# Kernel tuning notes

Measured on AMD Instinct MI355X. Metric: run time of the kernel, lower is better.

## Reference

```python
import jax, jax.numpy as jnp
import numpy as np

N, E = 50000, 800000
F_NODE, F_EDGE, H, LAT, MAXN = 128, 16, 128, 64, 200


def setup_inputs() -> dict:
    key = jax.random.key(0)
    ks = jax.random.split(key, 40)
    s = 0.05
    p = {
        'x': jax.random.normal(ks[0], (N, F_NODE), jnp.float32),
        'edge_index': jax.random.randint(ks[1], (2, E), 0, N, jnp.int64),
        'edge_attr': jax.random.normal(ks[2], (E, F_EDGE), jnp.float32),
        'eps': jax.random.normal(ks[3], (1, LAT), jnp.float32),
        'num_nodes': N,
        # GATConv layer 1 (heads=1)
        'W1': jax.random.normal(ks[4], (F_NODE, H), jnp.float32) * s,
        'att_src1': jax.random.normal(ks[5], (H,), jnp.float32) * s,
        'att_dst1': jax.random.normal(ks[6], (H,), jnp.float32) * s,
        'We1': jax.random.normal(ks[7], (F_EDGE, H), jnp.float32) * s,
        'att_e1': jax.random.normal(ks[8], (H,), jnp.float32) * s,
        'b1': jnp.zeros((H,), jnp.float32),
        # GATConv layer 2
        'W2': jax.random.normal(ks[9], (H, H), jnp.float32) * s,
        'att_src2': jax.random.normal(ks[10], (H,), jnp.float32) * s,
        'att_dst2': jax.random.normal(ks[11], (H,), jnp.float32) * s,
        'We2': jax.random.normal(ks[12], (F_EDGE, H), jnp.float32) * s,
        'att_e2': jax.random.normal(ks[13], (H,), jnp.float32) * s,
        'b2': jnp.zeros((H,), jnp.float32),
        # heads
        'mu_W': jax.random.normal(ks[14], (H, LAT), jnp.float32) * s,
        'mu_b': jnp.zeros((LAT,), jnp.float32),
        'lv_W': jax.random.normal(ks[15], (H, LAT), jnp.float32) * s,
        'lv_b': jnp.zeros((LAT,), jnp.float32),
        'dec_W': jax.random.normal(ks[16], (LAT, H), jnp.float32) * s,
        'dec_b': jnp.zeros((H,), jnp.float32),
        'adj_W1': jax.random.normal(ks[17], (H, H), jnp.float32) * s,
        'adj_b1': jnp.zeros((H,), jnp.float32),
        'adj_W2': jax.random.normal(ks[18], (H, MAXN), jnp.float32) * s,
        'adj_b2': jnp.zeros((MAXN,), jnp.float32),
        'nd_W1': jax.random.normal(ks[19], (H, H), jnp.float32) * s,
        'nd_b1': jnp.zeros((H,), jnp.float32),
        'nd_W2': jax.random.normal(ks[20], (H, F_NODE), jnp.float32) * s,
        'nd_b2': jnp.zeros((F_NODE,), jnp.float32),
    }
    return p


def _gat(h, src, dst, ea, W, a_s, a_d, We, a_e, b, n):
    # PyG GATConv, heads=1: linear transform, per-edge attention, segment softmax over dst
    g = h @ W                                     # [n, H]
    alpha = jax.nn.leaky_relu((g @ a_s)[src] + (g @ a_d)[dst] + (ea @ We) @ a_e,
                              negative_slope=0.2)  # [E']
    m = jax.ops.segment_max(alpha, dst, num_segments=n)
    ex = jnp.exp(alpha - m[dst])
    den = jax.ops.segment_sum(ex, dst, num_segments=n)
    w = ex / den[dst]
    return jax.ops.segment_sum(w[:, None] * g[src], dst, num_segments=n) + b


def _forward(x, edge_index, edge_attr, eps, num_nodes,
             W1, att_src1, att_dst1, We1, att_e1, b1,
             W2, att_src2, att_dst2, We2, att_e2, b2,
             mu_W, mu_b, lv_W, lv_b, dec_W, dec_b,
             adj_W1, adj_b1, adj_W2, adj_b2, nd_W1, nd_b1, nd_W2, nd_b2):
    n = x.shape[0]
    src, dst = edge_index[0], edge_index[1]
    # add self loops; self-loop edge_attr = per-node mean of incoming edge_attr (PyG fill_value='mean')
    deg = jax.ops.segment_sum(jnp.ones((src.shape[0],), x.dtype), dst, num_segments=n)
    mean_ea = jax.ops.segment_sum(edge_attr, dst, num_segments=n) / jnp.maximum(deg, 1.0)[:, None]
    loop = jnp.arange(n)
    src_f = jnp.concatenate([src, loop])
    dst_f = jnp.concatenate([dst, loop])
    ea_f = jnp.concatenate([edge_attr, mean_ea])
    h = jax.nn.relu(_gat(x, src_f, dst_f, ea_f, W1, att_src1, att_dst1, We1, att_e1, b1, n))
    h = jax.nn.relu(_gat(h, src_f, dst_f, ea_f, W2, att_src2, att_dst2, We2, att_e2, b2, n))
    hg = h.mean(axis=0, keepdims=True)            # global_mean_pool, single graph -> [1, H]
    mu = hg @ mu_W + mu_b
    logvar = hg @ lv_W + lv_b
    z = mu + eps * jnp.exp(0.5 * logvar)
    hd = jax.nn.relu(z @ dec_W + dec_b)           # [1, H]
    hn = jnp.broadcast_to(hd[:, None, :], (1, num_nodes, hd.shape[-1]))
    adj = jax.nn.relu(hn @ adj_W1 + adj_b1) @ adj_W2 + adj_b2   # [1, n, MAXN]
    adj = adj[:, :, :num_nodes]
    nodes = jax.nn.relu(hn @ nd_W1 + nd_b1) @ nd_W2 + nd_b2     # [1, n, F_NODE]
    return adj, nodes, mu, logvar


def reference(x, edge_index, edge_attr, eps, num_nodes,
              W1, att_src1, att_dst1, We1, att_e1, b1,
              W2, att_src2, att_dst2, We2, att_e2, b2,
              mu_W, mu_b, lv_W, lv_b, dec_W, dec_b,
              adj_W1, adj_b1, adj_W2, adj_b2, nd_W1, nd_b1, nd_W2, nd_b2):
    return _forward(x, edge_index, edge_attr, eps, num_nodes,
                    W1, att_src1, att_dst1, We1, att_e1, b1,
                    W2, att_src2, att_dst2, We2, att_e2, b2,
                    mu_W, mu_b, lv_W, lv_b, dec_W, dec_b,
                    adj_W1, adj_b1, adj_W2, adj_b2, nd_W1, nd_b1, nd_W2, nd_b2)
```

## Files before the change

### kernel.cpp

```cpp
#include <hip/hip_runtime.h>
#include <math.h>

#define NN   50000
#define EE   800000
#define EF   850000
#define HH   128
#define FE   16
#define LATD 64
#define MAXNN 200

#define ADJ_TOT   10000000
#define NODES_TOT 6400000
#define OUT_TOT   16400000
#define MU_OFF    16400000
#define LV_OFF    16400064

#define GEMMBLOCKS 782
#define DEGBLOCKS  3125

typedef __attribute__((ext_vector_type(8))) short bf16x8;
typedef __attribute__((ext_vector_type(4))) float f32x4;
typedef __attribute__((ext_vector_type(2))) float f32x2;

__device__ __forceinline__ unsigned short f2bf(float f){
  unsigned int u = __float_as_uint(f);
  unsigned int r = (u + 0x7FFFu + ((u>>16)&1u)) >> 16;
  return (unsigned short)r;
}
__device__ __forceinline__ float bf2f(unsigned short h){
  return __uint_as_float(((unsigned int)h)<<16);
}

__global__ __launch_bounds__(256) void kprep(int* ideg, float* hgsum,
                       const float* We1, const float* ae1, const float* We2, const float* ae2,
                       float* wa1, float* wa2,
                       const float* W1, const float* W2,
                       unsigned short* Wp1, unsigned short* Wp2){
  int i = blockIdx.x*256 + threadIdx.x;
  if(i < NN) ideg[i]=0;
  if(i < HH) hgsum[i]=0.f;
  if(i < FE){
    float s1=0.f, s2=0.f;
    for(int j=0;j<HH;j++){ s1 += We1[i*HH+j]*ae1[j]; s2 += We2[i*HH+j]*ae2[j]; }
    wa1[i]=s1; wa2[i]=s2;
  }
  if(i < HH*HH){
    int n = i >> 7, k = i & 127;
    Wp1[i] = f2bf(W1[k*HH + n]);
    Wp2[i] = f2bf(W2[k*HH + n]);
  }
}

__device__ __forceinline__ void gemm_body(int bid, int tid, const void* __restrict__ hin, int h_is_fp32,
    const unsigned short* __restrict__ Wp,
    const float* __restrict__ atts, const float* __restrict__ attd,
    unsigned char* __restrict__ A8, float* __restrict__ asrc, float* __restrict__ adst){
  int lane = tid & 63;
  int wid  = tid >> 6;
  int l = lane & 15, q = lane >> 4;
  int r0 = bid*64 + wid*16;
  if(r0 >= NN) return;
  const unsigned short* hb = (const unsigned short*)hin;
  const float*          hf = (const float*)hin;
  int row = r0 + l;

  f32x4 acc[8];
  #pragma unroll
  for(int t=0;t<8;t++) acc[t]=(f32x4){0.f,0.f,0.f,0.f};

  #pragma unroll
  for(int kb=0;kb<4;kb++){
    bf16x8 a;
    if(h_is_fp32){
      const float* p = hf + (size_t)row*HH + kb*32 + q*8;
      float4 u0 = *(const float4*)(p);
      float4 u1 = *(const float4*)(p+4);
      a[0]=(short)f2bf(u0.x); a[1]=(short)f2bf(u0.y); a[2]=(short)f2bf(u0.z); a[3]=(short)f2bf(u0.w);
      a[4]=(short)f2bf(u1.x); a[5]=(short)f2bf(u1.y); a[6]=(short)f2bf(u1.z); a[7]=(short)f2bf(u1.w);
    } else {
      a = *(const bf16x8*)(hb + (size_t)row*HH + kb*32 + q*8);
    }
    #pragma unroll
    for(int t=0;t<8;t++){
      bf16x8 b = *(const bf16x8*)(Wp + (size_t)(t*16+l)*HH + kb*32 + q*8);
      acc[t] = __builtin_amdgcn_mfma_f32_16x16x32_bf16(a, b, acc[t], 0,0,0);
    }
  }

  float av[8], dv[8];
  #pragma unroll
  for(int t=0;t<8;t++){ av[t]=atts[t*16+l]; dv[t]=attd[t*16+l]; }
  #pragma unroll
  for(int reg=0;reg<4;reg++){
    float ps=0.f, pd=0.f;
    #pragma unroll
    for(int t=0;t<8;t++){ ps+=acc[t][reg]*av[t]; pd+=acc[t][reg]*dv[t]; }
    #pragma unroll
    for(int m=8;m>=1;m>>=1){ ps+=__shfl_xor(ps,m,16); pd+=__shfl_xor(pd,m,16); }
    if(l==0){ int R=r0+q*4+reg; asrc[R]=ps; adst[R]=pd; }
  }
  #pragma unroll
  for(int t=0;t<8;t++)
    #pragma unroll
    for(int reg=0;reg<4;reg++){
      int pk = __builtin_amdgcn_cvt_pk_fp8_f32(acc[t][reg], 0.f, 0, false);
      A8[(size_t)(r0+q*4+reg)*HH + t*16 + l] = (unsigned char)(pk & 0xFF);
    }
}

__global__ __launch_bounds__(256) void kgemm3(const void* __restrict__ hin, int h_is_fp32,
    const unsigned short* __restrict__ Wp,
    const float* __restrict__ atts, const float* __restrict__ attd,
    unsigned char* __restrict__ A8, float* __restrict__ asrc, float* __restrict__ adst){
  gemm_body(blockIdx.x, threadIdx.x, hin, h_is_fp32, Wp, atts, attd, A8, asrc, adst);
}

__global__ __launch_bounds__(256) void kdeggemm(
    const int* __restrict__ ei, int* ideg, unsigned short* __restrict__ erank,
    const void* __restrict__ hin, int h_is_fp32,
    const unsigned short* __restrict__ Wp,
    const float* __restrict__ atts, const float* __restrict__ attd,
    unsigned char* __restrict__ A8, float* __restrict__ asrc, float* __restrict__ adst){
  if(blockIdx.x < GEMMBLOCKS){
    gemm_body(blockIdx.x, threadIdx.x, hin, h_is_fp32, Wp, atts, attd, A8, asrc, adst);
  } else {
    int e = (blockIdx.x - GEMMBLOCKS)*256 + threadIdx.x;
    if(e < EE) erank[e] = (unsigned short)atomicAdd(&ideg[ei[EE+e]], 1);
  }
}

__global__ void kscan1(const int* __restrict__ ideg, int* rowstart, int* blocksum){
  __shared__ int sd[1024];
  int t=threadIdx.x; int i=blockIdx.x*1024+t;
  int v = (i<NN)? (ideg[i]+1) : 0;
  sd[t]=v; __syncthreads();
  for(int off=1; off<1024; off<<=1){
    int x = (t>=off)? sd[t-off] : 0;
    __syncthreads();
    sd[t] += x;
    __syncthreads();
  }
  if(i<NN) rowstart[i] = sd[t]-v;
  if(t==1023) blocksum[blockIdx.x]=sd[1023];
}
__global__ __launch_bounds__(256) void kscan3i(int* rowstart, const int* __restrict__ blocksum, int nb){
  __shared__ int bo[64];
  int t = threadIdx.x;
  if(t < 64){
    int v = (t<nb)? blocksum[t] : 0;
    int inc = v;
    #pragma unroll
    for(int off=1; off<64; off<<=1){
      int x = __shfl_up(inc, off);
      if(t>=off) inc += x;
    }
    bo[t] = inc - v;
  }
  __syncthreads();
  int i = blockIdx.x*256 + t;
  if(i<NN) rowstart[i] += bo[i>>10];
  if(i==0) rowstart[NN] = bo[nb];
}

__device__ __forceinline__ unsigned etpack(const float4* a4,
                         const float* __restrict__ wa1, const float* __restrict__ wa2){
  float4 v0=a4[0], v1=a4[1], v2=a4[2], v3=a4[3];
  float va[16]={v0.x,v0.y,v0.z,v0.w, v1.x,v1.y,v1.z,v1.w,
                v2.x,v2.y,v2.z,v2.w, v3.x,v3.y,v3.z,v3.w};
  float d1=0.f,d2=0.f;
  #pragma unroll
  for(int f=0;f<FE;f++){ d1+=va[f]*wa1[f]; d2+=va[f]*wa2[f]; }
  return (unsigned)f2bf(d1) | ((unsigned)f2bf(d2)<<16);
}
__global__ __launch_bounds__(256) void kscatter(const int* __restrict__ ei, const float* __restrict__ ea,
                         const float* __restrict__ wa1, const float* __restrict__ wa2,
                         const int* __restrict__ rowstart, const unsigned short* __restrict__ erank,
                         uint2* __restrict__ csr){
  int e0 = (blockIdx.x*256 + threadIdx.x)*2;
  if(e0>=EE) return;
  int sA=ei[e0],    sB=ei[e0+1];
  int dA=ei[EE+e0], dB=ei[EE+e0+1];
  int rA=(int)erank[e0], rB=(int)erank[e0+1];
  int pA=rowstart[dA]+rA, pB=rowstart[dB]+rB;
  const float4* a4 = (const float4*)(ea + (size_t)e0*FE);
  unsigned yA = etpack(a4,   wa1, wa2);
  unsigned yB = etpack(a4+4, wa1, wa2);
  uint2 enA; enA.x=(unsigned)sA; enA.y=yA;
  uint2 enB; enB.x=(unsigned)sB; enB.y=yB;
  csr[pA]=enA; csr[pB]=enB;
}

__global__ __launch_bounds__(256) void kgat(const unsigned char* __restrict__ A8,
    const float* __restrict__ asrc, const float* __restrict__ adst,
    const int* __restrict__ rowstart, const uint2* __restrict__ csr,
    int etsel, const float* __restrict__ bias,
    float* __restrict__ alphabuf, int* __restrict__ srcbuf,
    unsigned short* __restrict__ Bout){
  int lane = threadIdx.x & 63;
  int wid  = threadIdx.x >> 6;
  int i = blockIdx.x*4 + wid;
  if(i >= NN) return;
  int base = rowstart[i];
  int len  = rowstart[i+1]-base;
  float adi = adst[i];
  int lq = lane & 15;
  int qq = lane >> 4;
  float av[8];
  #pragma unroll
  for(int j=0;j<8;j++) av[j]=0.f;

  if(__builtin_expect(len <= 64, 1)){
    int s = i; float et = 0.f;
    if(lane < len-1){
      uint2 en = csr[base+lane];
      s = (int)en.x;
      et = etsel ? bf2f((unsigned short)(en.y>>16)) : bf2f((unsigned short)(en.y & 0xFFFFu));
    }
    float ets = (lane < len-1) ? et : 0.f;
    #pragma unroll
    for(int mk=32;mk>=1;mk>>=1) ets += __shfl_xor(ets,mk);
    if(lane == len-1) et = ets / fmaxf((float)(len-1), 1.f);
    float a = -1e30f;
    if(lane < len){
      a = asrc[s] + adi + et;
      a = fmaxf(a, 0.2f*a);
    }
    float m = a;
    #pragma unroll
    for(int mk=32;mk>=1;mk>>=1) m = fmaxf(m, __shfl_xor(m,mk));
    float ex = (lane<len) ? __expf(a-m) : 0.f;
    float sm = ex;
    #pragma unroll
    for(int mk=32;mk>=1;mk>>=1) sm += __shfl_xor(sm,mk);
    ex *= __builtin_amdgcn_rcpf(sm);

    int P4 = (len+3)>>2;
    for(int t0=0; t0<P4; t0+=6){
      int skv[6]; float w[6];
      #pragma unroll
      for(int j=0;j<6;j++){
        if(t0+j < P4){
          int idx = 4*(t0+j) + qq;
          skv[j] = __shfl(s, idx);
          w[j]   = __shfl(ex, idx);
        } else { skv[j] = i; w[j] = 0.f; }
      }
      unsigned ux[6], uy[6];
      #pragma unroll
      for(int j=0;j<6;j++){
        uint2 u = *(const uint2*)(A8 + (size_t)skv[j]*HH + lq*8);
        ux[j]=u.x; uy[j]=u.y;
      }
      #pragma unroll
      for(int j=0;j<6;j++){
        f32x2 v;
        v=__builtin_amdgcn_cvt_pk_f32_fp8((int)ux[j],false); av[0]+=w[j]*v[0]; av[1]+=w[j]*v[1];
        v=__builtin_amdgcn_cvt_pk_f32_fp8((int)ux[j],true ); av[2]+=w[j]*v[0]; av[3]+=w[j]*v[1];
        v=__builtin_amdgcn_cvt_pk_f32_fp8((int)uy[j],false); av[4]+=w[j]*v[0]; av[5]+=w[j]*v[1];
        v=__builtin_amdgcn_cvt_pk_f32_fp8((int)uy[j],true ); av[6]+=w[j]*v[0]; av[7]+=w[j]*v[1];
      }
    }
  } else {
    int deg = len-1;
    float lm = -1e30f, ets = 0.f;
    for(int k=lane;k<deg;k+=64){
      uint2 en = csr[base+k];
      int sr = (int)en.x;
      float et = etsel ? bf2f((unsigned short)(en.y>>16)) : bf2f((unsigned short)(en.y & 0xFFFFu));
      ets += et;
      float a = asrc[sr] + adi + et;
      a = fmaxf(a, 0.2f*a);
      alphabuf[base+k]=a; srcbuf[base+k]=sr;
      lm = fmaxf(lm,a);
    }
    #pragma unroll
    for(int mk=32;mk>=1;mk>>=1){
      ets += __shfl_xor(ets,mk);
      lm   = fmaxf(lm, __shfl_xor(lm,mk));
    }
    float aself = asrc[i] + adi + ets/(float)deg;
    aself = fmaxf(aself, 0.2f*aself);
    lm = fmaxf(lm, aself);
    float ls=0.f;
    for(int k=lane;k<len;k+=64){
      float a = (k<deg)? alphabuf[base+k] : aself;
      float e_ = __expf(a-lm);
      alphabuf[base+k]=e_;
      ls += e_;
    }
    #pragma unroll
    for(int mk=32;mk>=1;mk>>=1) ls += __shfl_xor(ls,mk);
    float inv = 1.f/ls;
    int P4 = (len+3)>>2;
    for(int t=0;t<P4;t++){
      int k = 4*t + qq;
      int sk = i; float wk = 0.f;
      if(k<len){
        sk = (k<deg)? srcbuf[base+k] : i;
        wk = alphabuf[base+k]*inv;
      }
      uint2 u = *(const uint2*)(A8 + (size_t)sk*HH + lq*8);
      f32x2 v;
      v=__builtin_amdgcn_cvt_pk_f32_fp8((int)u.x,false); av[0]+=wk*v[0]; av[1]+=wk*v[1];
      v=__builtin_amdgcn_cvt_pk_f32_fp8((int)u.x,true ); av[2]+=wk*v[0]; av[3]+=wk*v[1];
      v=__builtin_amdgcn_cvt_pk_f32_fp8((int)u.y,false); av[4]+=wk*v[0]; av[5]+=wk*v[1];
      v=__builtin_amdgcn_cvt_pk_f32_fp8((int)u.y,true ); av[6]+=wk*v[0]; av[7]+=wk*v[1];
    }
  }

  #pragma unroll
  for(int j=0;j<8;j++){
    av[j] += __shfl_xor(av[j],16);
    av[j] += __shfl_xor(av[j],32);
  }
  if(qq==0){
    const float4* bp = (const float4*)(bias + lq*8);
    float4 b0=bp[0], b1=bp[1];
    float o0=fmaxf(av[0]+b0.x,0.f), o1=fmaxf(av[1]+b0.y,0.f);
    float o2=fmaxf(av[2]+b0.z,0.f), o3=fmaxf(av[3]+b0.w,0.f);
    float o4=fmaxf(av[4]+b1.x,0.f), o5=fmaxf(av[5]+b1.y,0.f);
    float o6=fmaxf(av[6]+b1.z,0.f), o7=fmaxf(av[7]+b1.w,0.f);
    uint4 ov;
    ov.x=(unsigned)f2bf(o0)|((unsigned)f2bf(o1)<<16);
    ov.y=(unsigned)f2bf(o2)|((unsigned)f2bf(o3)<<16);
    ov.z=(unsigned)f2bf(o4)|((unsigned)f2bf(o5)<<16);
    ov.w=(unsigned)f2bf(o6)|((unsigned)f2bf(o7)<<16);
    *(uint4*)(Bout + (size_t)i*HH + lq*8) = ov;
  }
}

__global__ __launch_bounds__(256) void khg(const unsigned short* __restrict__ B, float* hgsum){
  int f = threadIdx.x & 127;
  int half = threadIdx.x >> 7;
  float s=0.f;
  for(int i = blockIdx.x*2+half; i < NN; i += gridDim.x*2)
    s += bf2f(B[(size_t)i*HH + f]);
  __shared__ float sd[256];
  sd[threadIdx.x]=s; __syncthreads();
  if(half==0) atomicAdd(&hgsum[f], sd[threadIdx.x]+sd[threadIdx.x+128]);
}

__global__ __launch_bounds__(256) void kdec(const float* __restrict__ hgsum, const float* __restrict__ eps,
   const float* muW,const float* mub,const float* lvW,const float* lvb,
   const float* decW,const float* decb,
   const float* aW1,const float* ab1,const float* aW2,const float* ab2,
   const float* nW1,const float* nb1,const float* nW2,const float* nb2,
   float* out, float* rowadj, float* rownodes){
  __shared__ float hg[HH], z[LATD], hd[HH], t1[HH], t2[HH];
  int t=threadIdx.x;
  if(t<HH) hg[t]=hgsum[t]*(1.0f/NN);
  __syncthreads();
  if(t<LATD){
    float mu=mub[t], lv=lvb[t];
    #pragma unroll 8
    for(int k=0;k<HH;k++){ mu += hg[k]*muW[k*LATD+t]; lv += hg[k]*lvW[k*LATD+t]; }
    out[MU_OFF+t]=mu; out[LV_OFF+t]=lv;
    z[t]=mu + eps[t]*expf(0.5f*lv);
  }
  __syncthreads();
  if(t<HH){
    float a=decb[t];
    #pragma unroll 8
    for(int k=0;k<LATD;k++) a += z[k]*decW[k*HH+t];
    hd[t]=fmaxf(a,0.f);
  }
  __syncthreads();
  if(t<HH){
    float a=ab1[t];
    #pragma unroll 8
    for(int k=0;k<HH;k++) a += hd[k]*aW1[k*HH+t];
    t1[t]=fmaxf(a,0.f);
  } else {
    int j=t-HH;
    float a=nb1[j];
    #pragma unroll 8
    for(int k=0;k<HH;k++) a += hd[k]*nW1[k*HH+j];
    t2[j]=fmaxf(a,0.f);
  }
  __syncthreads();
  for(int j=t;j<MAXNN;j+=256){
    float a=ab2[j];
    #pragma unroll 8
    for(int k=0;k<HH;k++) a += t1[k]*aW2[k*MAXNN+j];
    rowadj[j]=a;
  }
  if(t<HH){
    float a=nb2[t];
    #pragma unroll 8
    for(int k=0;k<HH;k++) a += t2[k]*nW2[k*HH+t];
    rownodes[t]=a;
  }
}

__global__ __launch_bounds__(256) void kbcast(const float* __restrict__ rowadj,
                                              const float* __restrict__ rownodes,
                                              float* __restrict__ out){
  __shared__ float row[MAXNN+HH];
  int t=threadIdx.x;
  if(t<MAXNN) row[t]=rowadj[t];
  if(t<HH) row[MAXNN+t]=rownodes[t];
  __syncthreads();
  int stride=gridDim.x*blockDim.x;
  const int tot4 = OUT_TOT/4;
  for(int q=blockIdx.x*blockDim.x+t; q<tot4; q+=stride){
    int idx = q*4;
    float4 vv;
    if(idx<ADJ_TOT){
      int j = idx % MAXNN;
      vv = *(const float4*)&row[j];
    } else {
      int j = (idx-ADJ_TOT) & (HH-1);
      vv = *(const float4*)&row[MAXNN+j];
    }
    *(float4*)&out[idx] = vv;
  }
}

extern "C" void kernel_launch(void* const* d_in, const int* in_sizes, int n_in,
                              void* d_out, int out_size, void* d_ws, size_t ws_size,
                              hipStream_t stream){
  const float* x   = (const float*)d_in[0];
  const int*   ei  = (const int*)d_in[1];
  const float* ea  = (const float*)d_in[2];
  const float* eps = (const float*)d_in[3];
  const float* W1  =(const float*)d_in[5];
  const float* as1 =(const float*)d_in[6];
  const float* ad1 =(const float*)d_in[7];
  const float* We1 =(const float*)d_in[8];
  const float* ae1 =(const float*)d_in[9];
  const float* b1  =(const float*)d_in[10];
  const float* W2  =(const float*)d_in[11];
  const float* as2 =(const float*)d_in[12];
  const float* ad2 =(const float*)d_in[13];
  const float* We2 =(const float*)d_in[14];
  const float* ae2 =(const float*)d_in[15];
  const float* b2  =(const float*)d_in[16];
  const float* muW =(const float*)d_in[17];
  const float* mub =(const float*)d_in[18];
  const float* lvW =(const float*)d_in[19];
  const float* lvb =(const float*)d_in[20];
  const float* decW=(const float*)d_in[21];
  const float* decb=(const float*)d_in[22];
  const float* aW1 =(const float*)d_in[23];
  const float* ab1 =(const float*)d_in[24];
  const float* aW2 =(const float*)d_in[25];
  const float* ab2 =(const float*)d_in[26];
  const float* nW1 =(const float*)d_in[27];
  const float* nb1 =(const float*)d_in[28];
  const float* nW2 =(const float*)d_in[29];
  const float* nb2 =(const float*)d_in[30];
  float* out=(float*)d_out;

  char* w=(char*)d_ws;
  unsigned char*  A8  = (unsigned char*)w;  w += (size_t)NN*HH;
  unsigned short* Bbf = (unsigned short*)w; w += (size_t)NN*HH*2;
  unsigned short* Wp1 = (unsigned short*)w; w += (size_t)HH*HH*2;
  unsigned short* Wp2 = (unsigned short*)w; w += (size_t)HH*HH*2;
  uint2*  csr      = (uint2*)w;  w += (size_t)EF*8;
  float*  alphabuf = (float*)w;  w += (size_t)EF*4;
  int*    srcbuf   = (int*)w;    w += (size_t)EF*4;
  unsigned short* erank = (unsigned short*)w; w += (size_t)EE*2;
  int*    rowstart = (int*)w;    w += (size_t)(NN+1)*4;
  int*    ideg     = (int*)w;    w += (size_t)NN*4;
  float*  hgsum    = (float*)w;  w += 128*4;
  float*  asrc     = (float*)w;  w += (size_t)NN*4;
  float*  adst     = (float*)w;  w += (size_t)NN*4;
  float*  wa1      = (float*)w;  w += 16*4;
  float*  wa2      = (float*)w;  w += 16*4;
  float*  rowadj   = (float*)w;  w += 256*4;
  float*  rownodes = (float*)w;  w += 128*4;
  int*    blocksum = (int*)w;    w += 64*4;

  int nb = (NN+1023)/1024;
  int gatblocks  = (NN+3)/4;

  hipLaunchKernelGGL(kprep, dim3((NN+255)/256), dim3(256), 0, stream,
                     ideg, hgsum, We1, ae1, We2, ae2, wa1, wa2, W1, W2, Wp1, Wp2);
  hipLaunchKernelGGL(kdeggemm, dim3(GEMMBLOCKS+DEGBLOCKS), dim3(256), 0, stream,
                     ei, ideg, erank,
                     (const void*)x, 1, Wp1, as1, ad1, A8, asrc, adst);
  hipLaunchKernelGGL(kscan1, dim3(nb), dim3(1024), 0, stream, ideg, rowstart, blocksum);
  hipLaunchKernelGGL(kscan3i, dim3((NN+255)/256), dim3(256), 0, stream, rowstart, blocksum, nb);
  hipLaunchKernelGGL(kscatter, dim3((EE/2+255)/256), dim3(256), 0, stream,
                     ei, ea, wa1, wa2, rowstart, erank, csr);
  hipLaunchKernelGGL(kgat,  dim3(gatblocks), dim3(256), 0, stream,
                     A8, asrc, adst, rowstart, csr, 0, b1, alphabuf, srcbuf, Bbf);
  hipLaunchKernelGGL(kgemm3, dim3(GEMMBLOCKS), dim3(256), 0, stream,
                     (const void*)Bbf, 0, Wp2, as2, ad2, A8, asrc, adst);
  hipLaunchKernelGGL(kgat,  dim3(gatblocks), dim3(256), 0, stream,
                     A8, asrc, adst, rowstart, csr, 1, b2, alphabuf, srcbuf, Bbf);
  hipLaunchKernelGGL(khg,   dim3(512), dim3(256), 0, stream, Bbf, hgsum);
  hipLaunchKernelGGL(kdec,  dim3(1), dim3(256), 0, stream, hgsum, eps,
                     muW,mub,lvW,lvb,decW,decb,aW1,ab1,aW2,ab2,nW1,nb1,nW2,nb2,
                     out, rowadj, rownodes);
  hipLaunchKernelGGL(kbcast, dim3(2048), dim3(256), 0, stream, rowadj, rownodes, out);
}
```

Before: 404.7 us.

## Fold scan block-offset pass into consumers, vectorize degree atomics, preload GEMM A fragments

Removes the separate kscan3i kernel. Each consumer kernel (kscatter, kgat) now recomputes the block-offset prefix from blocksum in shared memory and adds it when reading rowstart. The degree-count blocks each handle four edges with a vectorized int4 load of destinations and a ushort4 store of ranks. The GEMM body loads all A fragments up front before the MFMA loop. The aim is to save one kernel launch and one pass over rowstart, and to raise memory-level parallelism. The cost is extra per-block prefix work and a __syncthreads in every kgat and kscatter block.

```diff
diff --git a/kernel.cpp b/kernel.cpp
--- a/kernel.cpp
+++ b/kernel.cpp
@@ -16,7 +16,8 @@
 #define LV_OFF    16400064
 
 #define GEMMBLOCKS 782
-#define DEGBLOCKS  3125
+#define DEGBLOCKS  782
+#define NBSCAN     49
 
 typedef __attribute__((ext_vector_type(8))) short bf16x8;
 typedef __attribute__((ext_vector_type(4))) float f32x4;
@@ -29,6 +30,20 @@
 }
 __device__ __forceinline__ float bf2f(unsigned short h){
   return __uint_as_float(((unsigned int)h)<<16);
+}
+
+__device__ __forceinline__ void load_bo(const int* __restrict__ blocksum, int* bo, int tid){
+  if(tid < 64){
+    int v = (tid < NBSCAN)? blocksum[tid] : 0;
+    int inc = v;
+    #pragma unroll
+    for(int off=1; off<64; off<<=1){
+      int x = __shfl_up(inc, off);
+      if(tid>=off) inc += x;
+    }
+    bo[tid] = inc - v;
+  }
+  __syncthreads();
 }
 
 __global__ __launch_bounds__(256) void kprep(int* ideg, float* hgsum,
@@ -64,26 +79,38 @@
   const float*          hf = (const float*)hin;
   int row = r0 + l;
 
+  bf16x8 afr[4];
+  if(h_is_fp32){
+    float4 u[8];
+    #pragma unroll
+    for(int kb=0;kb<4;kb++){
+      const float* p = hf + (size_t)row*HH + kb*32 + q*8;
+      u[kb*2]   = *(const float4*)(p);
+      u[kb*2+1] = *(const float4*)(p+4);
+    }
+    #pragma unroll
+    for(int kb=0;kb<4;kb++){
+      afr[kb][0]=(short)f2bf(u[kb*2].x);   afr[kb][1]=(short)f2bf(u[kb*2].y);
+      afr[kb][2]=(short)f2bf(u[kb*2].z);   afr[kb][3]=(short)f2bf(u[kb*2].w);
+      afr[kb][4]=(short)f2bf(u[kb*2+1].x); afr[kb][5]=(short)f2bf(u[kb*2+1].y);
+      afr[kb][6]=(short)f2bf(u[kb*2+1].z); afr[kb][7]=(short)f2bf(u[kb*2+1].w);
+    }
+  } else {
+    #pragma unroll
+    for(int kb=0;kb<4;kb++)
+      afr[kb] = *(const bf16x8*)(hb + (size_t)row*HH + kb*32 + q*8);
+  }
+
   f32x4 acc[8];
   #pragma unroll
   for(int t=0;t<8;t++) acc[t]=(f32x4){0.f,0.f,0.f,0.f};
 
   #pragma unroll
   for(int kb=0;kb<4;kb++){
-    bf16x8 a;
-    if(h_is_fp32){
-      const float* p = hf + (size_t)row*HH + kb*32 + q*8;
-      float4 u0 = *(const float4*)(p);
-      float4 u1 = *(const float4*)(p+4);
-      a[0]=(short)f2bf(u0.x); a[1]=(short)f2bf(u0.y); a[2]=(short)f2bf(u0.z); a[3]=(short)f2bf(u0.w);
-      a[4]=(short)f2bf(u1.x); a[5]=(short)f2bf(u1.y); a[6]=(short)f2bf(u1.z); a[7]=(short)f2bf(u1.w);
-    } else {
-      a = *(const bf16x8*)(hb + (size_t)row*HH + kb*32 + q*8);
-    }
     #pragma unroll
     for(int t=0;t<8;t++){
       bf16x8 b = *(const bf16x8*)(Wp + (size_t)(t*16+l)*HH + kb*32 + q*8);
-      acc[t] = __builtin_amdgcn_mfma_f32_16x16x32_bf16(a, b, acc[t], 0,0,0);
+      acc[t] = __builtin_amdgcn_mfma_f32_16x16x32_bf16(afr[kb], b, acc[t], 0,0,0);
     }
   }
 
@@ -124,8 +151,19 @@
   if(blockIdx.x < GEMMBLOCKS){
     gemm_body(blockIdx.x, threadIdx.x, hin, h_is_fp32, Wp, atts, attd, A8, asrc, adst);
   } else {
-    int e = (blockIdx.x - GEMMBLOCKS)*256 + threadIdx.x;
-    if(e < EE) erank[e] = (unsigned short)atomicAdd(&ideg[ei[EE+e]], 1);
+    int e0 = ((blockIdx.x - GEMMBLOCKS)*256 + threadIdx.x)*4;
+    if(e0 + 3 < EE){
+      int4 d4 = *(const int4*)(ei + EE + e0);
+      unsigned short r0 = (unsigned short)atomicAdd(&ideg[d4.x], 1);
+      unsigned short r1 = (unsigned short)atomicAdd(&ideg[d4.y], 1);
+      unsigned short r2 = (unsigned short)atomicAdd(&ideg[d4.z], 1);
+      unsigned short r3 = (unsigned short)atomicAdd(&ideg[d4.w], 1);
+      ushort4 rr; rr.x=r0; rr.y=r1; rr.z=r2; rr.w=r3;
+      *(ushort4*)(erank + e0) = rr;
+    } else {
+      for(int j=0;j<4;j++)
+        if(e0+j < EE) erank[e0+j] = (unsigned short)atomicAdd(&ideg[ei[EE+e0+j]], 1);
+    }
   }
 }
 
@@ -141,25 +179,8 @@
     __syncthreads();
   }
   if(i<NN) rowstart[i] = sd[t]-v;
+  else if(i==NN) rowstart[NN] = sd[t];
   if(t==1023) blocksum[blockIdx.x]=sd[1023];
-}
-__global__ __launch_bounds__(256) void kscan3i(int* rowstart, const int* __restrict__ blocksum, int nb){
-  __shared__ int bo[64];
-  int t = threadIdx.x;
-  if(t < 64){
-    int v = (t<nb)? blocksum[t] : 0;
-    int inc = v;
-    #pragma unroll
-    for(int off=1; off<64; off<<=1){
-      int x = __shfl_up(inc, off);
-      if(t>=off) inc += x;
-    }
-    bo[t] = inc - v;
-  }
-  __syncthreads();
-  int i = blockIdx.x*256 + t;
-  if(i<NN) rowstart[i] += bo[i>>10];
-  if(i==0) rowstart[NN] = bo[nb];
 }
 
 __device__ __forceinline__ unsigned etpack(const float4* a4,
@@ -174,14 +195,17 @@
 }
 __global__ __launch_bounds__(256) void kscatter(const int* __restrict__ ei, const float* __restrict__ ea,
                          const float* __restrict__ wa1, const float* __restrict__ wa2,
-                         const int* __restrict__ rowstart, const unsigned short* __restrict__ erank,
+                         const int* __restrict__ rowstart, const int* __restrict__ blocksum,
+                         const unsigned short* __restrict__ erank,
                          uint2* __restrict__ csr){
+  __shared__ int bo[64];
+  load_bo(blocksum, bo, threadIdx.x);
   int e0 = (blockIdx.x*256 + threadIdx.x)*2;
   if(e0>=EE) return;
   int sA=ei[e0],    sB=ei[e0+1];
   int dA=ei[EE+e0], dB=ei[EE+e0+1];
   int rA=(int)erank[e0], rB=(int)erank[e0+1];
-  int pA=rowstart[dA]+rA, pB=rowstart[dB]+rB;
+  int pA=rowstart[dA]+bo[dA>>10]+rA, pB=rowstart[dB]+bo[dB>>10]+rB;
   const float4* a4 = (const float4*)(ea + (size_t)e0*FE);
   unsigned yA = etpack(a4,   wa1, wa2);
   unsigned yB = etpack(a4+4, wa1, wa2);
@@ -192,16 +216,20 @@
 
 __global__ __launch_bounds__(256) void kgat(const unsigned char* __restrict__ A8,
     const float* __restrict__ asrc, const float* __restrict__ adst,
-    const int* __restrict__ rowstart, const uint2* __restrict__ csr,
+    const int* __restrict__ rowstart, const int* __restrict__ blocksum,
+    const uint2* __restrict__ csr,
     int etsel, const float* __restrict__ bias,
     float* __restrict__ alphabuf, int* __restrict__ srcbuf,
     unsigned short* __restrict__ Bout){
+  __shared__ int bo[64];
+  load_bo(blocksum, bo, threadIdx.x);
   int lane = threadIdx.x & 63;
   int wid  = threadIdx.x >> 6;
   int i = blockIdx.x*4 + wid;
   if(i >= NN) return;
-  int base = rowstart[i];
-  int len  = rowstart[i+1]-base;
+  int base = rowstart[i]   + bo[i>>10];
+  int end  = rowstart[i+1] + bo[(i+1)>>10];
+  int len  = end - base;
   float adi = adst[i];
   int lq = lane & 15;
   int qq = lane >> 4;
@@ -471,7 +499,6 @@
   float*  rownodes = (float*)w;  w += 128*4;
   int*    blocksum = (int*)w;    w += 64*4;
 
-  int nb = (NN+1023)/1024;
   int gatblocks  = (NN+3)/4;
 
   hipLaunchKernelGGL(kprep, dim3((NN+255)/256), dim3(256), 0, stream,
@@ -479,16 +506,15 @@
   hipLaunchKernelGGL(kdeggemm, dim3(GEMMBLOCKS+DEGBLOCKS), dim3(256), 0, stream,
                      ei, ideg, erank,
                      (const void*)x, 1, Wp1, as1, ad1, A8, asrc, adst);
-  hipLaunchKernelGGL(kscan1, dim3(nb), dim3(1024), 0, stream, ideg, rowstart, blocksum);
-  hipLaunchKernelGGL(kscan3i, dim3((NN+255)/256), dim3(256), 0, stream, rowstart, blocksum, nb);
+  hipLaunchKernelGGL(kscan1, dim3(NBSCAN), dim3(1024), 0, stream, ideg, rowstart, blocksum);
   hipLaunchKernelGGL(kscatter, dim3((EE/2+255)/256), dim3(256), 0, stream,
-                     ei, ea, wa1, wa2, rowstart, erank, csr);
+                     ei, ea, wa1, wa2, rowstart, blocksum, erank, csr);
   hipLaunchKernelGGL(kgat,  dim3(gatblocks), dim3(256), 0, stream,
-                     A8, asrc, adst, rowstart, csr, 0, b1, alphabuf, srcbuf, Bbf);
+                     A8, asrc, adst, rowstart, blocksum, csr, 0, b1, alphabuf, srcbuf, Bbf);
   hipLaunchKernelGGL(kgemm3, dim3(GEMMBLOCKS), dim3(256), 0, stream,
                      (const void*)Bbf, 0, Wp2, as2, ad2, A8, asrc, adst);
   hipLaunchKernelGGL(kgat,  dim3(gatblocks), dim3(256), 0, stream,
-                     A8, asrc, adst, rowstart, csr, 1, b2, alphabuf, srcbuf, Bbf);
+                     A8, asrc, adst, rowstart, blocksum, csr, 1, b2, alphabuf, srcbuf, Bbf);
   hipLaunchKernelGGL(khg,   dim3(512), dim3(256), 0, stream, Bbf, hgsum);
   hipLaunchKernelGGL(kdec,  dim3(1), dim3(256), 0, stream, hgsum, eps,
                      muW,mub,lvW,lvb,decW,decb,aW1,ab1,aW2,ab2,nW1,nb1,nW2,nb2,
```

Result: no change. 412.5 us (+1.9%).
